# Optimization experiments

Measured on AMD Instinct MI355X. Metric: run time of the kernel, lower is better.

The kernel has to match this reference:

```python
import jax, jax.numpy as jnp
import numpy as np

D_MODEL = 1024
N_HEADS = 16
D_FF = 4096
EPS = 1e-5


def setup_inputs() -> dict:
    key = jax.random.key(0)
    ks = jax.random.split(key, 16)
    s = 0.02
    d, f = D_MODEL, D_FF
    return {
        "x": jax.random.normal(ks[0], (4, 2048, d), dtype=jnp.float32),
        "WQ": jax.random.normal(ks[1], (d, d), dtype=jnp.float32) * s,
        "bQ": jnp.zeros((d,), dtype=jnp.float32),
        "WK": jax.random.normal(ks[2], (d, d), dtype=jnp.float32) * s,
        "bK": jnp.zeros((d,), dtype=jnp.float32),
        "WV": jax.random.normal(ks[3], (d, d), dtype=jnp.float32) * s,
        "bV": jnp.zeros((d,), dtype=jnp.float32),
        "WO": jax.random.normal(ks[4], (d, d), dtype=jnp.float32) * s,
        "bO": jnp.zeros((d,), dtype=jnp.float32),
        "W1": jax.random.normal(ks[5], (f, d), dtype=jnp.float32) * s,
        "b1": jnp.zeros((f,), dtype=jnp.float32),
        "W2": jax.random.normal(ks[6], (d, f), dtype=jnp.float32) * s,
        "b2": jnp.zeros((d,), dtype=jnp.float32),
        "g1": jnp.ones((d,), dtype=jnp.float32),
        "be1": jnp.zeros((d,), dtype=jnp.float32),
        "g2": jnp.ones((d,), dtype=jnp.float32),
        "be2": jnp.zeros((d,), dtype=jnp.float32),
    }


def _layernorm(x, g, b):
    mu = jnp.mean(x, axis=-1, keepdims=True)
    var = jnp.mean(jnp.square(x - mu), axis=-1, keepdims=True)
    return (x - mu) * jax.lax.rsqrt(var + EPS) * g + b


def reference(x, WQ, bQ, WK, bK, WV, bV, WO, bO, W1, b1, W2, b2, g1, be1, g2, be2):
    B, T, D = x.shape
    H, dk = N_HEADS, D // N_HEADS
    # projections (torch Linear: x @ W.T + b), reshape to [B,H,T,dk]
    q = (x @ WQ.T + bQ).reshape(B, T, H, dk).transpose(0, 2, 1, 3)
    k = (x @ WK.T + bK).reshape(B, T, H, dk).transpose(0, 2, 1, 3)
    v = (x @ WV.T + bV).reshape(B, T, H, dk).transpose(0, 2, 1, 3)
    scores = jnp.einsum("bhqd,bhkd->bhqk", q, k) / jnp.sqrt(jnp.float32(dk))
    causal = jnp.tril(jnp.ones((T, T), dtype=bool))
    scores = jnp.where(causal[None, None], scores, jnp.float32(-jnp.inf))
    attn = jax.nn.softmax(scores, axis=-1)
    out = jnp.einsum("bhqk,bhkd->bhqd", attn, v)
    out = out.transpose(0, 2, 1, 3).reshape(B, T, D)
    attn_out = out @ WO.T + bO
    x = _layernorm(x + attn_out, g1, be1)
    ff = jax.nn.relu(x @ W1.T + b1) @ W2.T + b2
    return _layernorm(x + ff, g2, be2)
```

## Files before the change

### kernel.cpp

```cpp
#include <hip/hip_runtime.h>

typedef unsigned short u16;
typedef unsigned int u32;
typedef __bf16 bf16x8 __attribute__((ext_vector_type(8)));
typedef float f32x4 __attribute__((ext_vector_type(4)));

__device__ __forceinline__ u16 f2bf(float f) {
  u32 u = __builtin_bit_cast(u32, f);
  u = (u + 0x7fffu + ((u >> 16) & 1u)) >> 16;
  return (u16)u;
}
__device__ __forceinline__ float bf2f(u16 h) {
  return __builtin_bit_cast(float, ((u32)h) << 16);
}

__device__ __forceinline__ void gll16(const u16* g, u16* l) {
  __builtin_amdgcn_global_load_lds((const __attribute__((address_space(1))) void*)g,
                                   (__attribute__((address_space(3))) void*)l, 16, 0, 0);
}

__device__ __forceinline__ void barrier() {
  asm volatile("" ::: "memory");
  __builtin_amdgcn_s_barrier();
  asm volatile("" ::: "memory");
}
__device__ __forceinline__ void waitv8() { asm volatile("s_waitcnt vmcnt(8)" ::: "memory"); }
__device__ __forceinline__ void waitv4() { asm volatile("s_waitcnt vmcnt(4)" ::: "memory"); }
__device__ __forceinline__ void waitv0() { asm volatile("s_waitcnt vmcnt(0)" ::: "memory"); }

__global__ __launch_bounds__(256) void cvt_all(const float* __restrict__ x,
                                               const float* __restrict__ WQ,
                                               const float* __restrict__ WK,
                                               const float* __restrict__ WV,
                                               const float* __restrict__ WO,
                                               const float* __restrict__ W1,
                                               const float* __restrict__ W2,
                                               u16* __restrict__ xb,
                                               u16* __restrict__ wqkvb,
                                               u16* __restrict__ wob,
                                               u16* __restrict__ w1b,
                                               u16* __restrict__ w2b) {
  const int S = 1 << 20;
  int i = (blockIdx.x * 256 + threadIdx.x) * 4;
  const float* src;
  u16* dst;
  if (i < 8 * S) { src = x + i; dst = xb + i; }
  else {
    int j = i - 8 * S;
    if (j < 3 * S)      { src = (j < S) ? WQ + j : (j < 2 * S) ? WK + (j - S) : WV + (j - 2 * S);
                          dst = wqkvb + j; }
    else if (j < 4 * S) { src = WO + (j - 3 * S); dst = wob + (j - 3 * S); }
    else if (j < 8 * S) { src = W1 + (j - 4 * S); dst = w1b + (j - 4 * S); }
    else                { src = W2 + (j - 8 * S); dst = w2b + (j - 8 * S); }
  }
  float4 v = *(const float4*)src;
  uint2 o;
  o.x = (u32)f2bf(v.x) | ((u32)f2bf(v.y) << 16);
  o.y = (u32)f2bf(v.z) | ((u32)f2bf(v.w) << 16);
  *(uint2*)dst = o;
}

template <int RELU, int QKV, int SPLIT>
__global__ __launch_bounds__(512, 2) void gemm256(const u16* __restrict__ A,
                                                  const u16* __restrict__ W,
                                                  const float* __restrict__ bias0,
                                                  void* __restrict__ C0,
                                                  int M, int N, int K,
                                                  const float* __restrict__ bias1,
                                                  void* __restrict__ C1,
                                                  const float* __restrict__ bias2,
                                                  void* __restrict__ C2,
                                                  int NBN) {
  __shared__ alignas(16) u16 lds[4 * 16384];
  const int tid = threadIdx.x;
  const int id = blockIdx.x;
  const int xcd = id & 7, r = id >> 3;
  int bm, bn, kz = 0, koff = 0, KL = K;
  if (SPLIT) {
    bn = (r & 3) << 8;
    const int q = r >> 2;
    bm = ((q & 3) * 8 + xcd) << 8;
    kz = q >> 2;
    KL = K >> 1;
    koff = kz * KL;
  } else {
    bn = (r % NBN) << 8;
    bm = ((r / NBN) * 8 + xcd) << 8;
  }
  const int wave = tid >> 6, lane = tid & 63;
  const int lr = lane & 15, quad = lane >> 4;
  const int wm = (wave >> 2) << 7;
  const int wn = (wave & 3) << 6;

  const int lrow = lane >> 2;
  const int lch = (lane & 3) ^ ((lane >> 3) & 3);
  const u16* Asrc = A + (size_t)(bm + wave * 16 + lrow) * K + koff + lch * 8;
  const u16* Wsrc = W + (size_t)(bn + wave * 16 + lrow) * K + koff + lch * 8;
  const size_t half = (size_t)128 * K;
  u16* dstbase = lds + wave * 512;

  const int NT = KL >> 5;
  const int fro = (quad ^ ((lr >> 1) & 3)) * 8;
  f32x4 acc[8][4] = {};

  #pragma unroll
  for (int t = 0; t < 3; t++) {
    u16* d = dstbase + t * 16384;
    gll16(Asrc + (size_t)t * 32, d);
    gll16(Asrc + (size_t)t * 32 + half, d + 4096);
    gll16(Wsrc + (size_t)t * 32, d + 8192);
    gll16(Wsrc + (size_t)t * 32 + half, d + 12288);
  }
  waitv8();
  barrier();

  for (int t = 0; t < NT; t++) {
    const u16* sa = lds + (t & 3) * 16384;
    const u16* sb = sa + 8192;
    const int tp = (t + 3 < NT) ? t + 3 : NT - 1;
    u16* d = dstbase + ((t + 3) & 3) * 16384;
    const size_t ko = (size_t)tp * 32;

    bf16x8 af[4], bfr[4];
    #pragma unroll
    for (int mi = 0; mi < 4; mi++)
      af[mi] = *(const bf16x8*)(sa + (wm + mi * 16 + lr) * 32 + fro);
    #pragma unroll
    for (int ni = 0; ni < 4; ni++)
      bfr[ni] = *(const bf16x8*)(sb + (wn + ni * 16 + lr) * 32 + fro);
    gll16(Asrc + ko, d);
    gll16(Asrc + ko + half, d + 4096);
    barrier();
    asm volatile("s_waitcnt lgkmcnt(0)" ::: "memory");
    __builtin_amdgcn_s_setprio(1);
    #pragma unroll
    for (int mi = 0; mi < 4; mi++)
      #pragma unroll
      for (int ni = 0; ni < 4; ni++)
        acc[mi][ni] = __builtin_amdgcn_mfma_f32_16x16x32_bf16(af[mi], bfr[ni], acc[mi][ni], 0, 0, 0);
    __builtin_amdgcn_s_setprio(0);
    barrier();

    #pragma unroll
    for (int mi = 0; mi < 4; mi++)
      af[mi] = *(const bf16x8*)(sa + (wm + 64 + mi * 16 + lr) * 32 + fro);
    gll16(Wsrc + ko, d + 8192);
    gll16(Wsrc + ko + half, d + 12288);
    barrier();
    asm volatile("s_waitcnt lgkmcnt(0)" ::: "memory");
    __builtin_amdgcn_s_setprio(1);
    #pragma unroll
    for (int mi = 0; mi < 4; mi++)
      #pragma unroll
      for (int ni = 0; ni < 4; ni++)
        acc[4 + mi][ni] = __builtin_amdgcn_mfma_f32_16x16x32_bf16(af[mi], bfr[ni], acc[4 + mi][ni], 0, 0, 0);
    __builtin_amdgcn_s_setprio(0);
    waitv8();
    barrier();
  }
  waitv0();

  const float* bp = bias0;
  void* outp = C0;
  float scale = 1.0f;
  int cb = bn, Nout = N, seg = 0;
  if (QKV) {
    Nout = 1024;
    seg = bn >> 10;
    cb = bn & 1023;
    if (seg == 0) scale = 0.125f * 1.44269504089f;
    else if (seg == 1) { bp = bias1; outp = C1; }
    else { bp = bias2; outp = C2; }
  }
  if (SPLIT && kz) outp = C1;

  if (QKV && seg == 2) {
    #pragma unroll
    for (int ni = 0; ni < 4; ni++) {
      const int col = cb + wn + ni * 16 + lr;
      const int hh = col >> 6, dl = col & 63;
      const float bv = bp[col];
      #pragma unroll
      for (int mi = 0; mi < 8; mi++) {
        const int row0 = bm + wm + mi * 16 + quad * 4;
        const int bb = row0 >> 11, tt = row0 & 2047;
        u16 pk[4];
        #pragma unroll
        for (int rg = 0; rg < 4; rg++) pk[rg] = f2bf(acc[mi][ni][rg] + bv);
        uint2 val;
        val.x = (u32)pk[0] | ((u32)pk[1] << 16);
        val.y = (u32)pk[2] | ((u32)pk[3] << 16);
        *(uint2*)(((u16*)outp) + ((size_t)((bb * 16 + hh) * 64 + dl)) * 2048 + tt) = val;
      }
    }
    return;
  }

  #pragma unroll
  for (int ni = 0; ni < 4; ni++) {
    const int col = cb + wn + ni * 16 + lr;
    const float bv = (SPLIT && kz) ? 0.0f : bp[col];
    #pragma unroll
    for (int mi = 0; mi < 8; mi++) {
      #pragma unroll
      for (int rg = 0; rg < 4; rg++) {
        int row = bm + wm + mi * 16 + quad * 4 + rg;
        float v = (acc[mi][ni][rg] + bv) * scale;
        if (RELU) v = fmaxf(v, 0.0f);
        ((u16*)outp)[(size_t)row * Nout + col] = f2bf(v);
      }
    }
  }
}

constexpr int ALD = 72;

__global__ __launch_bounds__(256) void attn_mfma(const u16* __restrict__ qb,
                                                 const u16* __restrict__ kb,
                                                 const u16* __restrict__ vt,
                                                 u16* __restrict__ ctxb, int T) {
  __shared__ alignas(16) u16 sK[2][64 * 64];
  __shared__ alignas(16) u16 sVt[2][64 * 64];
  __shared__ alignas(16) u16 sP[4 * 2 * 16 * ALD];
  const int tid = threadIdx.x;
  const int i = blockIdx.x;
  const int g = (i & 7) | (((i >> 7) & 7) << 3);
  const int p = (i >> 3) & 15;
  const int h = g >> 2, b = g & 3;
  const size_t base = ((size_t)(b * T)) * 1024 + h * 64;
  const size_t vbase = ((size_t)((b * 16 + h) * 64)) * T;
  const int lane = tid & 63, wave = tid >> 6;
  const int lr = lane & 15, quad = lane >> 4;
  u16* sPA = sP + (wave * 2) * 16 * ALD;
  u16* sPB = sPA + 16 * ALD;

  const int srow = lane >> 3;
  const int sch = ((lane & 7) ^ srow) * 8;
  const int fsw = lr & 7;

  const int qtA = 31 - p, qtB = p;

#define STAGEKV(ktt, slot) {                                                       \
    const int kc_ = ((ktt) <= qtA) ? (ktt) : qtA;                                  \
    _Pragma("unroll") for (int j_ = 0; j_ < 2; j_++) {                             \
      const int rb_ = (wave * 2 + j_) * 8;                                         \
      const int rr_ = rb_ + srow;                                                  \
      gll16(kb + base + (size_t)(kc_ * 64 + rr_) * 1024 + sch, sK[slot] + rb_ * 64);\
      gll16(vt + vbase + (size_t)rr_ * T + (size_t)(kc_ * 64) + sch, sVt[slot] + rb_ * 64);\
    } }

  const int q0A = qtA * 64 + wave * 16, q0B = qtB * 64 + wave * 16;
  bf16x8 qfA[2], qfB[2];
  #pragma unroll
  for (int sl = 0; sl < 2; sl++) {
    uint4 uA = *(const uint4*)(qb + base + (size_t)(q0A + lr) * 1024 + sl * 32 + quad * 8);
    qfA[sl] = __builtin_bit_cast(bf16x8, uA);
    uint4 uB = *(const uint4*)(qb + base + (size_t)(q0B + lr) * 1024 + sl * 32 + quad * 8);
    qfB[sl] = __builtin_bit_cast(bf16x8, uB);
  }
  f32x4 oA[4] = {}, oB[4] = {};
  float smA[4] = {0, 0, 0, 0}, smB[4] = {0, 0, 0, 0};

  STAGEKV(0, 0);

  for (int kt = 0; kt <= qtA; kt++) {
    const bool doB = (kt <= qtB);
    barrier();
    STAGEKV(kt + 1, (kt + 1) & 1);
    waitv4();
    barrier();
    const u16* sKc = sK[kt & 1];
    const u16* sVc = sVt[kt & 1];

    f32x4 sa[4] = {}, sb[4] = {};
    #pragma unroll
    for (int sl = 0; sl < 2; sl++) {
      bf16x8 kf[4];
      #pragma unroll
      for (int nt = 0; nt < 4; nt++)
        kf[nt] = *(const bf16x8*)(sKc + (nt * 16 + lr) * 64 + ((((sl << 2) | quad) ^ fsw) * 8));
      #pragma unroll
      for (int nt = 0; nt < 4; nt++)
        sa[nt] = __builtin_amdgcn_mfma_f32_16x16x32_bf16(kf[nt], qfA[sl], sa[nt], 0, 0, 0);
      if (doB) {
        #pragma unroll
        for (int nt = 0; nt < 4; nt++)
          sb[nt] = __builtin_amdgcn_mfma_f32_16x16x32_bf16(kf[nt], qfB[sl], sb[nt], 0, 0, 0);
      }
    }

    const int qloc = wave * 16 + lr;
    if (kt == qtA) {
      #pragma unroll
      for (int nt = 0; nt < 4; nt++)
        #pragma unroll
        for (int rg = 0; rg < 4; rg++)
          if (nt * 16 + quad * 4 + rg > qloc) sa[nt][rg] = -1e30f;
    }
    if (doB && kt == qtB) {
      #pragma unroll
      for (int nt = 0; nt < 4; nt++)
        #pragma unroll
        for (int rg = 0; rg < 4; rg++)
          if (nt * 16 + quad * 4 + rg > qloc) sb[nt][rg] = -1e30f;
    }

    #pragma unroll
    for (int nt = 0; nt < 4; nt++) {
      float e0 = __builtin_amdgcn_exp2f(sa[nt][0]);
      float e1 = __builtin_amdgcn_exp2f(sa[nt][1]);
      float e2 = __builtin_amdgcn_exp2f(sa[nt][2]);
      float e3 = __builtin_amdgcn_exp2f(sa[nt][3]);
      smA[nt] += (e0 + e1) + (e2 + e3);
      uint2 pk;
      pk.x = __builtin_amdgcn_perm(__builtin_bit_cast(u32, e1), __builtin_bit_cast(u32, e0), 0x07060302u);
      pk.y = __builtin_amdgcn_perm(__builtin_bit_cast(u32, e3), __builtin_bit_cast(u32, e2), 0x07060302u);
      *(uint2*)(sPA + lr * ALD + nt * 16 + quad * 4) = pk;
    }
    if (doB) {
      #pragma unroll
      for (int nt = 0; nt < 4; nt++) {
        float e0 = __builtin_amdgcn_exp2f(sb[nt][0]);
        float e1 = __builtin_amdgcn_exp2f(sb[nt][1]);
        float e2 = __builtin_amdgcn_exp2f(sb[nt][2]);
        float e3 = __builtin_amdgcn_exp2f(sb[nt][3]);
        smB[nt] += (e0 + e1) + (e2 + e3);
        uint2 pk;
        pk.x = __builtin_amdgcn_perm(__builtin_bit_cast(u32, e1), __builtin_bit_cast(u32, e0), 0x07060302u);
        pk.y = __builtin_amdgcn_perm(__builtin_bit_cast(u32, e3), __builtin_bit_cast(u32, e2), 0x07060302u);
        *(uint2*)(sPB + lr * ALD + nt * 16 + quad * 4) = pk;
      }
    }
    asm volatile("" ::: "memory");

    #pragma unroll
    for (int sl = 0; sl < 2; sl++) {
      bf16x8 vf[4];
      #pragma unroll
      for (int nt = 0; nt < 4; nt++)
        vf[nt] = *(const bf16x8*)(sVc + (nt * 16 + lr) * 64 + ((((sl << 2) | quad) ^ fsw) * 8));
      bf16x8 pfA = *(const bf16x8*)(sPA + lr * ALD + sl * 32 + quad * 8);
      #pragma unroll
      for (int nt = 0; nt < 4; nt++)
        oA[nt] = __builtin_amdgcn_mfma_f32_16x16x32_bf16(pfA, vf[nt], oA[nt], 0, 0, 0);
      if (doB) {
        bf16x8 pfB = *(const bf16x8*)(sPB + lr * ALD + sl * 32 + quad * 8);
        #pragma unroll
        for (int nt = 0; nt < 4; nt++)
          oB[nt] = __builtin_amdgcn_mfma_f32_16x16x32_bf16(pfB, vf[nt], oB[nt], 0, 0, 0);
      }
    }
  }
  waitv0();
#undef STAGEKV

  float sumA = (smA[0] + smA[1]) + (smA[2] + smA[3]);
  sumA += __shfl_xor(sumA, 16);
  sumA += __shfl_xor(sumA, 32);
  float sumB = (smB[0] + smB[1]) + (smB[2] + smB[3]);
  sumB += __shfl_xor(sumB, 16);
  sumB += __shfl_xor(sumB, 32);
  float invA[4], invB[4];
  #pragma unroll
  for (int rg = 0; rg < 4; rg++) {
    invA[rg] = 1.0f / __shfl(sumA, quad * 4 + rg);
    invB[rg] = 1.0f / __shfl(sumB, quad * 4 + rg);
  }
  #pragma unroll
  for (int nt = 0; nt < 4; nt++)
    #pragma unroll
    for (int rg = 0; rg < 4; rg++) {
      int qrow = q0A + quad * 4 + rg;
      ctxb[base + (size_t)qrow * 1024 + nt * 16 + lr] = f2bf(oA[nt][rg] * invA[rg]);
    }
  #pragma unroll
  for (int nt = 0; nt < 4; nt++)
    #pragma unroll
    for (int rg = 0; rg < 4; rg++) {
      int qrow = q0B + quad * 4 + rg;
      ctxb[base + (size_t)qrow * 1024 + nt * 16 + lr] = f2bf(oB[nt][rg] * invB[rg]);
    }
}

template <int ABF>
__global__ __launch_bounds__(256) void ln_kernel(const void* __restrict__ a,
                                                 const u16* __restrict__ b,
                                                 const u16* __restrict__ c,
                                                 const float* __restrict__ g,
                                                 const float* __restrict__ be,
                                                 float* __restrict__ of32,
                                                 u16* __restrict__ obf) {
  const int row = blockIdx.x;
  const int tid = threadIdx.x;
  const size_t base = (size_t)row * 1024;
  const int cc = tid * 4;
  float a0, a1, a2, a3;
  if (ABF) {
    uint2 ua = *(const uint2*)((const u16*)a + base + cc);
    a0 = bf2f(ua.x & 0xffff); a1 = bf2f(ua.x >> 16);
    a2 = bf2f(ua.y & 0xffff); a3 = bf2f(ua.y >> 16);
  } else {
    float4 xa = *(const float4*)((const float*)a + base + cc);
    a0 = xa.x; a1 = xa.y; a2 = xa.z; a3 = xa.w;
  }
  uint2 ub = *(const uint2*)(b + base + cc);
  uint2 uc = *(const uint2*)(c + base + cc);
  float v0 = a0 + bf2f(ub.x & 0xffff) + bf2f(uc.x & 0xffff);
  float v1 = a1 + bf2f(ub.x >> 16)    + bf2f(uc.x >> 16);
  float v2 = a2 + bf2f(ub.y & 0xffff) + bf2f(uc.y & 0xffff);
  float v3 = a3 + bf2f(ub.y >> 16)    + bf2f(uc.y >> 16);
  float s1 = v0 + v1 + v2 + v3;
  float s2 = v0 * v0 + v1 * v1 + v2 * v2 + v3 * v3;
  for (int off = 1; off < 64; off <<= 1) {
    s1 += __shfl_xor(s1, off);
    s2 += __shfl_xor(s2, off);
  }
  __shared__ float red[8];
  int wv = tid >> 6;
  if ((tid & 63) == 0) { red[wv] = s1; red[4 + wv] = s2; }
  __syncthreads();
  s1 = red[0] + red[1] + red[2] + red[3];
  s2 = red[4] + red[5] + red[6] + red[7];
  float mu = s1 * (1.0f / 1024.0f);
  float var = s2 * (1.0f / 1024.0f) - mu * mu;
  float rs = rsqrtf(var + 1e-5f);
  float4 gv = *(const float4*)(g + cc);
  float4 bev = *(const float4*)(be + cc);
  float y0 = (v0 - mu) * rs * gv.x + bev.x;
  float y1 = (v1 - mu) * rs * gv.y + bev.y;
  float y2 = (v2 - mu) * rs * gv.z + bev.z;
  float y3 = (v3 - mu) * rs * gv.w + bev.w;
  if (of32) {
    float4 o = make_float4(y0, y1, y2, y3);
    *(float4*)(of32 + base + cc) = o;
  }
  if (obf) {
    uint2 o;
    o.x = (u32)f2bf(y0) | ((u32)f2bf(y1) << 16);
    o.y = (u32)f2bf(y2) | ((u32)f2bf(y3) << 16);
    *(uint2*)(obf + base + cc) = o;
  }
}

extern "C" void kernel_launch(void* const* d_in, const int* in_sizes, int n_in,
                              void* d_out, int out_size, void* d_ws, size_t ws_size,
                              hipStream_t stream) {
  const int Mtok = 8192, D = 1024, F = 4096, T = 2048;
  const float* x   = (const float*)d_in[0];
  const float* WQ  = (const float*)d_in[1];
  const float* bQ  = (const float*)d_in[2];
  const float* WK  = (const float*)d_in[3];
  const float* bK  = (const float*)d_in[4];
  const float* WV  = (const float*)d_in[5];
  const float* bV  = (const float*)d_in[6];
  const float* WO  = (const float*)d_in[7];
  const float* bO  = (const float*)d_in[8];
  const float* W1  = (const float*)d_in[9];
  const float* b1  = (const float*)d_in[10];
  const float* W2  = (const float*)d_in[11];
  const float* b2  = (const float*)d_in[12];
  const float* g1  = (const float*)d_in[13];
  const float* be1 = (const float*)d_in[14];
  const float* g2  = (const float*)d_in[15];
  const float* be2 = (const float*)d_in[16];

  char* ws = (char*)d_ws;
  const size_t MB = 1024 * 1024;
  u16*  xb     = (u16*)(ws + 0);
  u16*  wqkvb  = (u16*)(ws + 16 * MB);
  u16*  wob    = (u16*)(ws + 22 * MB);
  u16*  w1b    = (u16*)(ws + 24 * MB);
  u16*  w2b    = (u16*)(ws + 32 * MB);
  u16*  qb     = (u16*)(ws + 40 * MB);
  u16*  kb     = (u16*)(ws + 56 * MB);
  u16*  vtb    = (u16*)(ws + 72 * MB);
  u16*  ctxb   = (u16*)(ws + 88 * MB);
  u16*  wp0    = (u16*)(ws + 104 * MB);
  u16*  wp1    = (u16*)(ws + 120 * MB);
  u16*  h1b    = (u16*)(ws + 136 * MB);
  u16*  ff1b   = (u16*)(ws + 40 * MB);
  u16*  fp0    = (u16*)(ws + 0);
  u16*  fp1    = (u16*)(ws + 16 * MB);
  float* out   = (float*)d_out;

  dim3 blk(256);
  dim3 blk512(512);
  cvt_all<<<(20 << 20) / 1024, blk, 0, stream>>>(x, WQ, WK, WV, WO, W1, W2,
                                                 xb, wqkvb, wob, w1b, w2b);

  gemm256<0, 1, 0><<<dim3(384), blk512, 0, stream>>>(xb, wqkvb, bQ, qb, Mtok, 3072, D,
                                                     bK, kb, bV, vtb, 12);
  attn_mfma<<<dim3(1024), blk, 0, stream>>>(qb, kb, vtb, ctxb, T);

  gemm256<0, 0, 1><<<dim3(256), blk512, 0, stream>>>(ctxb, wob, bO, wp0, Mtok, D, D,
                                                     nullptr, wp1, nullptr, nullptr, 4);
  ln_kernel<0><<<Mtok, blk, 0, stream>>>(x, wp0, wp1, g1, be1, nullptr, h1b);

  gemm256<1, 0, 0><<<dim3(512), blk512, 0, stream>>>(h1b, w1b, b1, ff1b, Mtok, F, D,
                                                     nullptr, nullptr, nullptr, nullptr, 16);
  gemm256<0, 0, 1><<<dim3(256), blk512, 0, stream>>>(ff1b, w2b, b2, fp0, Mtok, D, F,
                                                     nullptr, fp1, nullptr, nullptr, 4);
  ln_kernel<1><<<Mtok, blk, 0, stream>>>(h1b, fp0, fp1, g2, be2, out, (u16*)nullptr);
}
```

Before: 504.7 us.

## Rework causal attention with 32x32x16 MFMA and register-resident P via permlane swap

The attention kernel switches from 16x16x32 MFMAs, where each wave handled 16 rows of both paired query tiles, to 32x32x16 MFMAs where each wave owns 32 rows of a single query tile. The probability matrix is now repacked in registers with v_permlane32_swap instead of a round trip through LDS, which removes the sP shared buffer and its writes and reads. A rotation (vw) spreads the short and long tiles across waves. The risk is load imbalance: waves on the short tile sit idle at barriers while the loop runs to qtA, and register pressure goes up with 32-float tiles.

```diff
diff --git a/kernel.cpp b/kernel.cpp
--- a/kernel.cpp
+++ b/kernel.cpp
@@ -4,6 +4,7 @@
 typedef unsigned int u32;
 typedef __bf16 bf16x8 __attribute__((ext_vector_type(8)));
 typedef float f32x4 __attribute__((ext_vector_type(4)));
+typedef float f32x16 __attribute__((ext_vector_type(16)));
 
 __device__ __forceinline__ u16 f2bf(float f) {
   u32 u = __builtin_bit_cast(u32, f);
@@ -213,15 +214,12 @@
   }
 }
 
-constexpr int ALD = 72;
-
 __global__ __launch_bounds__(256) void attn_mfma(const u16* __restrict__ qb,
                                                  const u16* __restrict__ kb,
                                                  const u16* __restrict__ vt,
                                                  u16* __restrict__ ctxb, int T) {
   __shared__ alignas(16) u16 sK[2][64 * 64];
   __shared__ alignas(16) u16 sVt[2][64 * 64];
-  __shared__ alignas(16) u16 sP[4 * 2 * 16 * ALD];
   const int tid = threadIdx.x;
   const int i = blockIdx.x;
   const int g = (i & 7) | (((i >> 7) & 7) << 3);
@@ -230,15 +228,15 @@
   const size_t base = ((size_t)(b * T)) * 1024 + h * 64;
   const size_t vbase = ((size_t)((b * 16 + h) * 64)) * T;
   const int lane = tid & 63, wave = tid >> 6;
-  const int lr = lane & 15, quad = lane >> 4;
-  u16* sPA = sP + (wave * 2) * 16 * ALD;
-  u16* sPB = sPA + 16 * ALD;
+  const int l31 = lane & 31, hh = lane >> 5;
 
   const int srow = lane >> 3;
   const int sch = ((lane & 7) ^ srow) * 8;
-  const int fsw = lr & 7;
 
   const int qtA = 31 - p, qtB = p;
+  const int vw = (wave + (i & 3)) & 3;
+  const int myqt = (vw >> 1) ? qtB : qtA;
+  const int q0w = myqt * 64 + (vw & 1) * 32;
 
 #define STAGEKV(ktt, slot) {                                                       \
     const int kc_ = ((ktt) <= qtA) ? (ktt) : qtA;                                  \
@@ -249,137 +247,95 @@
       gll16(vt + vbase + (size_t)rr_ * T + (size_t)(kc_ * 64) + sch, sVt[slot] + rb_ * 64);\
     } }
 
-  const int q0A = qtA * 64 + wave * 16, q0B = qtB * 64 + wave * 16;
-  bf16x8 qfA[2], qfB[2];
+  bf16x8 qf[4];
   #pragma unroll
-  for (int sl = 0; sl < 2; sl++) {
-    uint4 uA = *(const uint4*)(qb + base + (size_t)(q0A + lr) * 1024 + sl * 32 + quad * 8);
-    qfA[sl] = __builtin_bit_cast(bf16x8, uA);
-    uint4 uB = *(const uint4*)(qb + base + (size_t)(q0B + lr) * 1024 + sl * 32 + quad * 8);
-    qfB[sl] = __builtin_bit_cast(bf16x8, uB);
-  }
-  f32x4 oA[4] = {}, oB[4] = {};
-  float smA[4] = {0, 0, 0, 0}, smB[4] = {0, 0, 0, 0};
+  for (int ds = 0; ds < 4; ds++) {
+    uint4 uq = *(const uint4*)(qb + base + (size_t)(q0w + l31) * 1024 + ds * 16 + hh * 8);
+    qf[ds] = __builtin_bit_cast(bf16x8, uq);
+  }
+  f32x16 o0 = {}, o1 = {};
+  float rsum = 0.0f;
+  const int fs8 = (l31 & 7);
 
   STAGEKV(0, 0);
 
   for (int kt = 0; kt <= qtA; kt++) {
-    const bool doB = (kt <= qtB);
     barrier();
     STAGEKV(kt + 1, (kt + 1) & 1);
     waitv4();
     barrier();
-    const u16* sKc = sK[kt & 1];
-    const u16* sVc = sVt[kt & 1];
-
-    f32x4 sa[4] = {}, sb[4] = {};
-    #pragma unroll
-    for (int sl = 0; sl < 2; sl++) {
-      bf16x8 kf[4];
-      #pragma unroll
-      for (int nt = 0; nt < 4; nt++)
-        kf[nt] = *(const bf16x8*)(sKc + (nt * 16 + lr) * 64 + ((((sl << 2) | quad) ^ fsw) * 8));
-      #pragma unroll
-      for (int nt = 0; nt < 4; nt++)
-        sa[nt] = __builtin_amdgcn_mfma_f32_16x16x32_bf16(kf[nt], qfA[sl], sa[nt], 0, 0, 0);
-      if (doB) {
+    if (kt <= myqt) {
+      const u16* sKc = sK[kt & 1];
+      const u16* sVc = sVt[kt & 1];
+
+      f32x16 s0v = {}, s1v = {};
+      #pragma unroll
+      for (int ds = 0; ds < 4; ds++) {
+        const int co = ((2 * ds + hh) ^ fs8) * 8;
+        bf16x8 kf0 = *(const bf16x8*)(sKc + l31 * 64 + co);
+        bf16x8 kf1 = *(const bf16x8*)(sKc + (32 + l31) * 64 + co);
+        s0v = __builtin_amdgcn_mfma_f32_32x32x16_bf16(kf0, qf[ds], s0v, 0, 0, 0);
+        s1v = __builtin_amdgcn_mfma_f32_32x32x16_bf16(kf1, qf[ds], s1v, 0, 0, 0);
+      }
+
+      if (kt == myqt) {
+        const int qloc = ((vw & 1) << 5) + l31;
         #pragma unroll
-        for (int nt = 0; nt < 4; nt++)
-          sb[nt] = __builtin_amdgcn_mfma_f32_16x16x32_bf16(kf[nt], qfB[sl], sb[nt], 0, 0, 0);
-      }
-    }
-
-    const int qloc = wave * 16 + lr;
-    if (kt == qtA) {
-      #pragma unroll
-      for (int nt = 0; nt < 4; nt++)
+        for (int rg = 0; rg < 16; rg++) {
+          const int key = (rg & 3) + 8 * (rg >> 2) + 4 * hh;
+          if (key > qloc) s0v[rg] = -1e30f;
+          if (key + 32 > qloc) s1v[rg] = -1e30f;
+        }
+      }
+
+      float e[32];
+      #pragma unroll
+      for (int rg = 0; rg < 16; rg++) {
+        e[rg] = __builtin_amdgcn_exp2f(s0v[rg]);
+        e[16 + rg] = __builtin_amdgcn_exp2f(s1v[rg]);
+        rsum += e[rg] + e[16 + rg];
+      }
+
+      union PW { u32 w[4]; bf16x8 v; } pf[4];
+      #pragma unroll
+      for (int t = 0; t < 2; t++) {
         #pragma unroll
-        for (int rg = 0; rg < 4; rg++)
-          if (nt * 16 + quad * 4 + rg > qloc) sa[nt][rg] = -1e30f;
-    }
-    if (doB && kt == qtB) {
-      #pragma unroll
-      for (int nt = 0; nt < 4; nt++)
-        #pragma unroll
-        for (int rg = 0; rg < 4; rg++)
-          if (nt * 16 + quad * 4 + rg > qloc) sb[nt][rg] = -1e30f;
-    }
-
-    #pragma unroll
-    for (int nt = 0; nt < 4; nt++) {
-      float e0 = __builtin_amdgcn_exp2f(sa[nt][0]);
-      float e1 = __builtin_amdgcn_exp2f(sa[nt][1]);
-      float e2 = __builtin_amdgcn_exp2f(sa[nt][2]);
-      float e3 = __builtin_amdgcn_exp2f(sa[nt][3]);
-      smA[nt] += (e0 + e1) + (e2 + e3);
-      uint2 pk;
-      pk.x = __builtin_amdgcn_perm(__builtin_bit_cast(u32, e1), __builtin_bit_cast(u32, e0), 0x07060302u);
-      pk.y = __builtin_amdgcn_perm(__builtin_bit_cast(u32, e3), __builtin_bit_cast(u32, e2), 0x07060302u);
-      *(uint2*)(sPA + lr * ALD + nt * 16 + quad * 4) = pk;
-    }
-    if (doB) {
-      #pragma unroll
-      for (int nt = 0; nt < 4; nt++) {
-        float e0 = __builtin_amdgcn_exp2f(sb[nt][0]);
-        float e1 = __builtin_amdgcn_exp2f(sb[nt][1]);
-        float e2 = __builtin_amdgcn_exp2f(sb[nt][2]);
-        float e3 = __builtin_amdgcn_exp2f(sb[nt][3]);
-        smB[nt] += (e0 + e1) + (e2 + e3);
-        uint2 pk;
-        pk.x = __builtin_amdgcn_perm(__builtin_bit_cast(u32, e1), __builtin_bit_cast(u32, e0), 0x07060302u);
-        pk.y = __builtin_amdgcn_perm(__builtin_bit_cast(u32, e3), __builtin_bit_cast(u32, e2), 0x07060302u);
-        *(uint2*)(sPB + lr * ALD + nt * 16 + quad * 4) = pk;
-      }
-    }
-    asm volatile("" ::: "memory");
-
-    #pragma unroll
-    for (int sl = 0; sl < 2; sl++) {
-      bf16x8 vf[4];
-      #pragma unroll
-      for (int nt = 0; nt < 4; nt++)
-        vf[nt] = *(const bf16x8*)(sVc + (nt * 16 + lr) * 64 + ((((sl << 2) | quad) ^ fsw) * 8));
-      bf16x8 pfA = *(const bf16x8*)(sPA + lr * ALD + sl * 32 + quad * 8);
-      #pragma unroll
-      for (int nt = 0; nt < 4; nt++)
-        oA[nt] = __builtin_amdgcn_mfma_f32_16x16x32_bf16(pfA, vf[nt], oA[nt], 0, 0, 0);
-      if (doB) {
-        bf16x8 pfB = *(const bf16x8*)(sPB + lr * ALD + sl * 32 + quad * 8);
-        #pragma unroll
-        for (int nt = 0; nt < 4; nt++)
-          oB[nt] = __builtin_amdgcn_mfma_f32_16x16x32_bf16(pfB, vf[nt], oB[nt], 0, 0, 0);
+        for (int sl = 0; sl < 2; sl++) {
+          const int rb = t * 16 + sl * 8;
+          u32 wa = __builtin_amdgcn_perm(__builtin_bit_cast(u32, e[rb + 1]), __builtin_bit_cast(u32, e[rb + 0]), 0x07060302u);
+          u32 wb = __builtin_amdgcn_perm(__builtin_bit_cast(u32, e[rb + 5]), __builtin_bit_cast(u32, e[rb + 4]), 0x07060302u);
+          u32 wc = __builtin_amdgcn_perm(__builtin_bit_cast(u32, e[rb + 3]), __builtin_bit_cast(u32, e[rb + 2]), 0x07060302u);
+          u32 wd = __builtin_amdgcn_perm(__builtin_bit_cast(u32, e[rb + 7]), __builtin_bit_cast(u32, e[rb + 6]), 0x07060302u);
+          asm("v_permlane32_swap_b32 %0, %1" : "+v"(wa), "+v"(wb));
+          asm("v_permlane32_swap_b32 %0, %1" : "+v"(wc), "+v"(wd));
+          pf[t * 2 + sl].w[0] = wa; pf[t * 2 + sl].w[1] = wc;
+          pf[t * 2 + sl].w[2] = wb; pf[t * 2 + sl].w[3] = wd;
+        }
+      }
+
+      #pragma unroll
+      for (int s = 0; s < 4; s++) {
+        const int co = ((2 * s + hh) ^ fs8) * 8;
+        bf16x8 vf0 = *(const bf16x8*)(sVc + l31 * 64 + co);
+        bf16x8 vf1 = *(const bf16x8*)(sVc + (32 + l31) * 64 + co);
+        o0 = __builtin_amdgcn_mfma_f32_32x32x16_bf16(pf[s].v, vf0, o0, 0, 0, 0);
+        o1 = __builtin_amdgcn_mfma_f32_32x32x16_bf16(pf[s].v, vf1, o1, 0, 0, 0);
       }
     }
   }
   waitv0();
 #undef STAGEKV
 
-  float sumA = (smA[0] + smA[1]) + (smA[2] + smA[3]);
-  sumA += __shfl_xor(sumA, 16);
-  sumA += __shfl_xor(sumA, 32);
-  float sumB = (smB[0] + smB[1]) + (smB[2] + smB[3]);
-  sumB += __shfl_xor(sumB, 16);
-  sumB += __shfl_xor(sumB, 32);
-  float invA[4], invB[4];
+  rsum += __shfl_xor(rsum, 32);
+  float inv = 1.0f / rsum;
   #pragma unroll
-  for (int rg = 0; rg < 4; rg++) {
-    invA[rg] = 1.0f / __shfl(sumA, quad * 4 + rg);
-    invB[rg] = 1.0f / __shfl(sumB, quad * 4 + rg);
-  }
-  #pragma unroll
-  for (int nt = 0; nt < 4; nt++)
-    #pragma unroll
-    for (int rg = 0; rg < 4; rg++) {
-      int qrow = q0A + quad * 4 + rg;
-      ctxb[base + (size_t)qrow * 1024 + nt * 16 + lr] = f2bf(oA[nt][rg] * invA[rg]);
-    }
-  #pragma unroll
-  for (int nt = 0; nt < 4; nt++)
-    #pragma unroll
-    for (int rg = 0; rg < 4; rg++) {
-      int qrow = q0B + quad * 4 + rg;
-      ctxb[base + (size_t)qrow * 1024 + nt * 16 + lr] = f2bf(oB[nt][rg] * invB[rg]);
-    }
+  for (int rg = 0; rg < 16; rg++) {
+    const int qr = (rg & 3) + 8 * (rg >> 2) + 4 * hh;
+    float iv = __shfl(inv, qr);
+    const size_t rowoff = base + (size_t)(q0w + qr) * 1024;
+    ctxb[rowoff + l31] = f2bf(o0[rg] * iv);
+    ctxb[rowoff + 32 + l31] = f2bf(o1[rg] * iv);
+  }
 }
 
 template <int ABF>
```

After: 503.9 us. No clear change (-0.2%).
